# Performance work log

Measured on AMD Instinct MI355X. Metric: run time of the kernel, lower is better.

Reference implementation:

```python
import jax, jax.numpy as jnp
import numpy as np

EPS = 1e-6

def _rms_norm(x, w):
    # x: [..., C], w: [C]
    return x * jax.lax.rsqrt(jnp.mean(x * x, axis=-1, keepdims=True) + EPS) * w


def setup_inputs() -> dict:
    key = jax.random.key(0)
    ks = jax.random.split(key, 8)
    N, E, H, C = 50000, 400000, 8, 32
    q = jax.random.normal(ks[0], (N, H, C), dtype=jnp.float32)
    k = jax.random.normal(ks[1], (N, H, C), dtype=jnp.float32)
    v = jax.random.normal(ks[2], (N, H, C), dtype=jnp.float32)
    e = jax.random.normal(ks[3], (E, H, C), dtype=jnp.float32)
    w_q_norm = jnp.ones((C,), dtype=jnp.float32)
    w_k_norm = jnp.ones((C,), dtype=jnp.float32)
    edge_src = jax.random.randint(ks[4], (E,), 0, N, dtype=jnp.int32)
    edge_dst = jnp.sort(jax.random.randint(ks[5], (E,), 0, N, dtype=jnp.int32))
    return {"q": q, "k": k, "v": v, "e": e, "w_q_norm": w_q_norm,
            "w_k_norm": w_k_norm, "edge_src": edge_src, "edge_dst": edge_dst}


def reference(q, k, v, e, w_q_norm, w_k_norm, edge_src, edge_dst):
    # q: [N_dst,H,C]; k,v: [N_src,H,C]; e: [E,H,C]
    N_dst, H, C = q.shape
    qk_scale = 1.0 / jnp.sqrt(jnp.float32(C))
    qn = _rms_norm(q, w_q_norm)          # fused RMSNorm on Q
    kn = _rms_norm(k, w_k_norm)          # fused RMSNorm on K
    ke = kn[edge_src] + e                # [E,H,C]
    ve = v[edge_src] + e                 # [E,H,C]
    s = jnp.einsum('ehc,ehc->eh', qn[edge_dst], ke) * qk_scale  # [E,H]
    # segment (per-destination) numerically-stable softmax == online softmax
    m = jax.ops.segment_max(s, edge_dst, num_segments=N_dst)     # [N_dst,H]
    m_safe = jnp.where(jnp.isfinite(m), m, 0.0)                  # empty dsts
    p = jnp.exp(s - m_safe[edge_dst])                            # [E,H]
    l = jax.ops.segment_sum(p, edge_dst, num_segments=N_dst)     # [N_dst,H]
    acc = jax.ops.segment_sum(p[..., None] * ve, edge_dst, num_segments=N_dst)
    out = jnp.where(l[..., None] > 0, acc / jnp.maximum(l, 1e-30)[..., None], 0.0)
    return out
```

## Files before the change

### kernel.cpp

```cpp
#include <hip/hip_runtime.h>
#include <math.h>


#define Hh 8
#define Cc 32
#define HC 256
#define EPSf 1e-6f

__global__ __launch_bounds__(64) void gt_attn_kernel(
    const float* __restrict__ q,
    const float* __restrict__ k,
    const float* __restrict__ v,
    const float* __restrict__ e,
    const float* __restrict__ wq,
    const float* __restrict__ wk,
    const int*   __restrict__ edge_src,
    const int*   __restrict__ edge_dst,
    float*       __restrict__ out,
    int N, int E)
{
    const int d   = blockIdx.x;
    const int tid = threadIdx.x;
    const int cq  = (tid & 7) * 4;

    int lo = 0, r = E;
    while (lo < r) { int mid = (lo + r) >> 1; if (edge_dst[mid] < d) lo = mid + 1; else r = mid; }
    int hi = lo; r = E;
    while (hi < r) { int mid = (hi + r) >> 1; if (edge_dst[mid] <= d) hi = mid + 1; else r = mid; }

    const float4 wq4 = *(const float4*)(wq + cq);
    const float4 wk4 = *(const float4*)(wk + cq);

    const float4 q4 = *(const float4*)(q + (size_t)d * HC + tid * 4);
    float ss = q4.x*q4.x + q4.y*q4.y + q4.z*q4.z + q4.w*q4.w;
    ss += __shfl_xor(ss, 1); ss += __shfl_xor(ss, 2); ss += __shfl_xor(ss, 4);
    const float qrs = rsqrtf(ss * (1.0f / Cc) + EPSf);
    float4 qn;
    qn.x = q4.x * qrs * wq4.x; qn.y = q4.y * qrs * wq4.y;
    qn.z = q4.z * qrs * wq4.z; qn.w = q4.w * qrs * wq4.w;

    const float qk_scale = rsqrtf((float)Cc);

    float m = -INFINITY, l = 0.0f;
    float4 acc = make_float4(0.f, 0.f, 0.f, 0.f);

    for (int ei = lo; ei < hi; ++ei) {
        const int src = edge_src[ei];
        const float4 k4 = *(const float4*)(k + (size_t)src * HC + tid * 4);
        float ks = k4.x*k4.x + k4.y*k4.y + k4.z*k4.z + k4.w*k4.w;
        ks += __shfl_xor(ks, 1); ks += __shfl_xor(ks, 2); ks += __shfl_xor(ks, 4);
        const float krs = rsqrtf(ks * (1.0f / Cc) + EPSf);

        const float4 e4 = *(const float4*)(e + (size_t)ei * HC + tid * 4);
        float4 ke;
        ke.x = k4.x * krs * wk4.x + e4.x;
        ke.y = k4.y * krs * wk4.y + e4.y;
        ke.z = k4.z * krs * wk4.z + e4.z;
        ke.w = k4.w * krs * wk4.w + e4.w;

        float s = qn.x*ke.x + qn.y*ke.y + qn.z*ke.z + qn.w*ke.w;
        s += __shfl_xor(s, 1); s += __shfl_xor(s, 2); s += __shfl_xor(s, 4);
        s *= qk_scale;

        const float m_new = fmaxf(m, s);
        const float alpha = __expf(m - m_new);
        const float p     = __expf(s - m_new);
        l = l * alpha + p;

        const float4 v4 = *(const float4*)(v + (size_t)src * HC + tid * 4);
        acc.x = acc.x * alpha + p * (v4.x + e4.x);
        acc.y = acc.y * alpha + p * (v4.y + e4.y);
        acc.z = acc.z * alpha + p * (v4.z + e4.z);
        acc.w = acc.w * alpha + p * (v4.w + e4.w);
        m = m_new;
    }

    float4 o;
    if (l > 0.0f) {
        const float inv = 1.0f / l;
        o.x = acc.x * inv; o.y = acc.y * inv; o.z = acc.z * inv; o.w = acc.w * inv;
    } else {
        o = make_float4(0.f, 0.f, 0.f, 0.f);
    }
    *(float4*)(out + (size_t)d * HC + tid * 4) = o;
}

extern "C" void kernel_launch(void* const* d_in, const int* in_sizes, int n_in,
                              void* d_out, int out_size, void* d_ws, size_t ws_size,
                              hipStream_t stream) {
    const float* q   = (const float*)d_in[0];
    const float* k   = (const float*)d_in[1];
    const float* v   = (const float*)d_in[2];
    const float* e   = (const float*)d_in[3];
    const float* wq  = (const float*)d_in[4];
    const float* wk  = (const float*)d_in[5];
    const int* esrc  = (const int*)d_in[6];
    const int* edst  = (const int*)d_in[7];
    float* out       = (float*)d_out;

    const int E  = in_sizes[6];
    const int hc = in_sizes[3] / E;
    const int N  = in_sizes[0] / hc;

    gt_attn_kernel<<<dim3(N), dim3(64), 0, stream>>>(q, k, v, e, wq, wk, esrc, edst, out, N, E);
}
```

Measured before the change: 710.1 us.

## Precompute CSR offsets and K norms, unroll edge loop by two

Splits the kernel into three launches. One builds per-destination CSR offsets once instead of running two binary searches per block. One precomputes a per-node, per-head K RMS scale so it is not recomputed for every edge. The main kernel packs four destinations per 256-thread block, processes edges two at a time to raise memory-level parallelism, and uses nontemporal loads for e and a nontemporal store for the output. The cost is two extra launches and some workspace traffic, plus an extra scattered load of kscale per edge.

Measured after the change: 706.3 us. No clear change (-0.5%).

```diff
diff --git a/kernel.cpp b/kernel.cpp
--- a/kernel.cpp
+++ b/kernel.cpp
@@ -7,82 +7,116 @@
 #define HC 256
 #define EPSf 1e-6f
 
-__global__ __launch_bounds__(64) void gt_attn_kernel(
+typedef float v4f __attribute__((ext_vector_type(4)));
+
+__global__ __launch_bounds__(256) void build_offs(
+    const int* __restrict__ edst, int* __restrict__ offs, int N, int E)
+{
+    int d = blockIdx.x * 256 + threadIdx.x;
+    if (d > N) return;
+    int lo = 0, r = E;
+    while (lo < r) { int mid = (lo + r) >> 1; if (edst[mid] < d) lo = mid + 1; else r = mid; }
+    offs[d] = lo;
+}
+
+__global__ __launch_bounds__(256) void build_kscale(
+    const float* __restrict__ k, float* __restrict__ kscale, int N)
+{
+    const int wave = threadIdx.x >> 6, lane = threadIdx.x & 63;
+    const int n = blockIdx.x * 4 + wave;
+    if (n >= N) return;
+    const v4f k4 = *(const v4f*)(k + (size_t)n * HC + lane * 4);
+    float ss = k4.x*k4.x + k4.y*k4.y + k4.z*k4.z + k4.w*k4.w;
+    ss += __shfl_xor(ss, 1); ss += __shfl_xor(ss, 2); ss += __shfl_xor(ss, 4);
+    if ((lane & 7) == 0)
+        kscale[n * Hh + (lane >> 3)] = rsqrtf(ss * (1.0f / Cc) + EPSf);
+}
+
+__global__ __launch_bounds__(256) void gt_attn_main(
     const float* __restrict__ q,
     const float* __restrict__ k,
     const float* __restrict__ v,
     const float* __restrict__ e,
     const float* __restrict__ wq,
     const float* __restrict__ wk,
-    const int*   __restrict__ edge_src,
-    const int*   __restrict__ edge_dst,
+    const int*   __restrict__ esrc,
+    const int*   __restrict__ offs,
+    const float* __restrict__ kscale,
     float*       __restrict__ out,
-    int N, int E)
+    int N)
 {
-    const int d   = blockIdx.x;
-    const int tid = threadIdx.x;
-    const int cq  = (tid & 7) * 4;
+    const int wave = threadIdx.x >> 6, lane = threadIdx.x & 63;
+    const int d = blockIdx.x * 4 + wave;
+    if (d >= N) return;
+    const int h  = lane >> 3;
+    const int cq = (lane & 7) * 4;
 
-    int lo = 0, r = E;
-    while (lo < r) { int mid = (lo + r) >> 1; if (edge_dst[mid] < d) lo = mid + 1; else r = mid; }
-    int hi = lo; r = E;
-    while (hi < r) { int mid = (hi + r) >> 1; if (edge_dst[mid] <= d) hi = mid + 1; else r = mid; }
+    const int lo = offs[d], hi = offs[d + 1];
 
-    const float4 wq4 = *(const float4*)(wq + cq);
-    const float4 wk4 = *(const float4*)(wk + cq);
+    const v4f wq4 = *(const v4f*)(wq + cq);
+    const v4f wk4 = *(const v4f*)(wk + cq);
 
-    const float4 q4 = *(const float4*)(q + (size_t)d * HC + tid * 4);
+    const v4f q4 = *(const v4f*)(q + (size_t)d * HC + lane * 4);
     float ss = q4.x*q4.x + q4.y*q4.y + q4.z*q4.z + q4.w*q4.w;
     ss += __shfl_xor(ss, 1); ss += __shfl_xor(ss, 2); ss += __shfl_xor(ss, 4);
-    const float qrs = rsqrtf(ss * (1.0f / Cc) + EPSf);
-    float4 qn;
-    qn.x = q4.x * qrs * wq4.x; qn.y = q4.y * qrs * wq4.y;
-    qn.z = q4.z * qrs * wq4.z; qn.w = q4.w * qrs * wq4.w;
+    const v4f qn = q4 * (rsqrtf(ss * (1.0f / Cc) + EPSf)) * wq4;
 
     const float qk_scale = rsqrtf((float)Cc);
 
     float m = -INFINITY, l = 0.0f;
-    float4 acc = make_float4(0.f, 0.f, 0.f, 0.f);
+    v4f acc = {0.f, 0.f, 0.f, 0.f};
 
-    for (int ei = lo; ei < hi; ++ei) {
-        const int src = edge_src[ei];
-        const float4 k4 = *(const float4*)(k + (size_t)src * HC + tid * 4);
-        float ks = k4.x*k4.x + k4.y*k4.y + k4.z*k4.z + k4.w*k4.w;
-        ks += __shfl_xor(ks, 1); ks += __shfl_xor(ks, 2); ks += __shfl_xor(ks, 4);
-        const float krs = rsqrtf(ks * (1.0f / Cc) + EPSf);
+    int ei = lo;
+    for (; ei + 1 < hi; ei += 2) {
+        const int s0 = esrc[ei], s1 = esrc[ei + 1];
+        const v4f ka = *(const v4f*)(k + (size_t)s0 * HC + lane * 4);
+        const v4f kb = *(const v4f*)(k + (size_t)s1 * HC + lane * 4);
+        const v4f ea = __builtin_nontemporal_load((const v4f*)(e + (size_t)ei * HC + lane * 4));
+        const v4f eb = __builtin_nontemporal_load((const v4f*)(e + (size_t)(ei + 1) * HC + lane * 4));
+        const v4f va = *(const v4f*)(v + (size_t)s0 * HC + lane * 4);
+        const v4f vb = *(const v4f*)(v + (size_t)s1 * HC + lane * 4);
+        const float krsa = kscale[s0 * Hh + h];
+        const float krsb = kscale[s1 * Hh + h];
 
-        const float4 e4 = *(const float4*)(e + (size_t)ei * HC + tid * 4);
-        float4 ke;
-        ke.x = k4.x * krs * wk4.x + e4.x;
-        ke.y = k4.y * krs * wk4.y + e4.y;
-        ke.z = k4.z * krs * wk4.z + e4.z;
-        ke.w = k4.w * krs * wk4.w + e4.w;
+        const v4f kea = ka * krsa * wk4 + ea;
+        const v4f keb = kb * krsb * wk4 + eb;
 
-        float s = qn.x*ke.x + qn.y*ke.y + qn.z*ke.z + qn.w*ke.w;
-        s += __shfl_xor(s, 1); s += __shfl_xor(s, 2); s += __shfl_xor(s, 4);
-        s *= qk_scale;
+        float sa = qn.x*kea.x + qn.y*kea.y + qn.z*kea.z + qn.w*kea.w;
+        float sb = qn.x*keb.x + qn.y*keb.y + qn.z*keb.z + qn.w*keb.w;
+        sa += __shfl_xor(sa, 1); sb += __shfl_xor(sb, 1);
+        sa += __shfl_xor(sa, 2); sb += __shfl_xor(sb, 2);
+        sa += __shfl_xor(sa, 4); sb += __shfl_xor(sb, 4);
+        sa *= qk_scale; sb *= qk_scale;
 
-        const float m_new = fmaxf(m, s);
-        const float alpha = __expf(m - m_new);
-        const float p     = __expf(s - m_new);
-        l = l * alpha + p;
-
-        const float4 v4 = *(const float4*)(v + (size_t)src * HC + tid * 4);
-        acc.x = acc.x * alpha + p * (v4.x + e4.x);
-        acc.y = acc.y * alpha + p * (v4.y + e4.y);
-        acc.z = acc.z * alpha + p * (v4.z + e4.z);
-        acc.w = acc.w * alpha + p * (v4.w + e4.w);
-        m = m_new;
+        const float mn = fmaxf(m, fmaxf(sa, sb));
+        const float al = __expf(m - mn);
+        const float pa = __expf(sa - mn);
+        const float pb = __expf(sb - mn);
+        l = l * al + pa + pb;
+        acc = acc * al + pa * (va + ea) + pb * (vb + eb);
+        m = mn;
+    }
+    if (ei < hi) {
+        const int s0 = esrc[ei];
+        const v4f ka = *(const v4f*)(k + (size_t)s0 * HC + lane * 4);
+        const v4f ea = __builtin_nontemporal_load((const v4f*)(e + (size_t)ei * HC + lane * 4));
+        const v4f va = *(const v4f*)(v + (size_t)s0 * HC + lane * 4);
+        const float krsa = kscale[s0 * Hh + h];
+        const v4f kea = ka * krsa * wk4 + ea;
+        float sa = qn.x*kea.x + qn.y*kea.y + qn.z*kea.z + qn.w*kea.w;
+        sa += __shfl_xor(sa, 1); sa += __shfl_xor(sa, 2); sa += __shfl_xor(sa, 4);
+        sa *= qk_scale;
+        const float mn = fmaxf(m, sa);
+        const float al = __expf(m - mn);
+        const float pa = __expf(sa - mn);
+        l = l * al + pa;
+        acc = acc * al + pa * (va + ea);
+        m = mn;
     }
 
-    float4 o;
-    if (l > 0.0f) {
-        const float inv = 1.0f / l;
-        o.x = acc.x * inv; o.y = acc.y * inv; o.z = acc.z * inv; o.w = acc.w * inv;
-    } else {
-        o = make_float4(0.f, 0.f, 0.f, 0.f);
-    }
-    *(float4*)(out + (size_t)d * HC + tid * 4) = o;
+    v4f o = {0.f, 0.f, 0.f, 0.f};
+    if (l > 0.0f) o = acc * (1.0f / l);
+    __builtin_nontemporal_store(o, (v4f*)(out + (size_t)d * HC + lane * 4));
 }
 
 extern "C" void kernel_launch(void* const* d_in, const int* in_sizes, int n_in,
@@ -102,5 +136,11 @@
     const int hc = in_sizes[3] / E;
     const int N  = in_sizes[0] / hc;
 
-    gt_attn_kernel<<<dim3(N), dim3(64), 0, stream>>>(q, k, v, e, wq, wk, esrc, edst, out, N, E);
+    int*   offs   = (int*)d_ws;
+    float* kscale = (float*)((char*)d_ws + ((size_t)(N + 1) * sizeof(int) + 255 & ~(size_t)255));
+
+    build_offs  <<<dim3((N + 256) / 256), dim3(256), 0, stream>>>(edst, offs, N, E);
+    build_kscale<<<dim3((N + 3) / 4),     dim3(256), 0, stream>>>(k, kscale, N);
+    gt_attn_main<<<dim3((N + 3) / 4),     dim3(256), 0, stream>>>(
+        q, k, v, e, wq, wk, esrc, offs, kscale, out, N);
 }
```
